# Kernel tuning notes

Hardware: AMD Instinct MI355X
Metric: run time of the kernel (lower is better)

## Reference

```python
import math
import jax, jax.numpy as jnp
import numpy as np

SCALING = 16.0 / 32.0  # alpha / rank


def real_fourier_orthogonal_multiply(c):
    """Vectorized equivalent of the per-frequency Python loop: build a complex
    spectrum from real Fourier coefficients and inverse-rfft along last dim."""
    n = c.shape[-1]
    sqrt_n = math.sqrt(n)
    pair_scale = math.sqrt(n / 2.0)
    max_f = (n - 1) // 2
    work = c.astype(jnp.float32)
    dc = (work[..., 0] * sqrt_n)[..., None].astype(jnp.complex64)
    cos = work[..., 1:1 + 2 * max_f:2] * pair_scale
    sin = work[..., 2:2 + 2 * max_f:2] * pair_scale
    mid = (cos - 1j * sin).astype(jnp.complex64)  # freqs 1..max_f
    parts = [dc, mid]
    if n % 2 == 0:
        parts.append((work[..., -1] * sqrt_n)[..., None].astype(jnp.complex64))
    spectrum = jnp.concatenate(parts, axis=-1)  # [..., n//2+1]
    return jnp.fft.irfft(spectrum, n=n, axis=-1).astype(c.dtype)


def setup_inputs() -> dict:
    key = jax.random.key(0)
    ks = jax.random.split(key, 9)
    B, S, D_in, D_out, R0, R1, E = 4, 2048, 4096, 4096, 32, 8, 3
    x = jax.random.normal(ks[0], (B, S, D_in), dtype=jnp.float32)
    W_base = jax.random.normal(ks[1], (D_out, D_in), dtype=jnp.float32) * 0.02
    b_base = jax.random.normal(ks[2], (D_out,), dtype=jnp.float32) * 0.02
    enc0 = jax.random.normal(ks[3], (R0, D_in), dtype=jnp.float32) * 0.02
    enc1 = jax.random.normal(ks[4], (R1, D_in), dtype=jnp.float32) * 0.02
    coefs0 = jax.random.normal(ks[5], (E, D_out, R0), dtype=jnp.float32) * 0.02
    coefs1 = jax.random.normal(ks[6], (E, D_out, R1), dtype=jnp.float32) * 0.02
    # sparse decoder masks (buffers in the torch module)
    mask0 = jax.random.randint(ks[7], (E, D_out, R0), 0, 2).astype(bool)
    mask1 = jax.random.randint(ks[8], (E, D_out, R1), 0, 2).astype(bool)
    return dict(x=x, W_base=W_base, b_base=b_base, enc0=enc0, enc1=enc1,
                coefs0=coefs0, coefs1=coefs1, mask0=mask0, mask1=mask1)


def reference(x, W_base, b_base, enc0, enc1, coefs0, coefs1, mask0, mask1):
    # base linear
    base = jnp.einsum('bsd,od->bso', x, W_base) + b_base
    # encoder blocks (shared across experts)
    e0 = jnp.einsum('bsd,rd->bsr', x, enc0)  # [B,S,R0]
    e1 = jnp.einsum('bsd,rd->bsr', x, enc1)  # [B,S,R1]
    # masked decoder blocks per expert, summed over blocks
    w0 = coefs0 * mask0.astype(coefs0.dtype)  # [E,O,R0]
    w1 = coefs1 * mask1.astype(coefs1.dtype)  # [E,O,R1]
    decoded = (jnp.einsum('bsr,eor->ebso', e0, w0)
               + jnp.einsum('bsr,eor->ebso', e1, w1))  # [E,B,S,O]
    transformed = real_fourier_orthogonal_multiply(decoded)
    update = transformed.sum(axis=0)  # sum over active experts
    return base + update * SCALING
```

## Files before the change

### kernel.cpp

```cpp
#include <hip/hip_runtime.h>

typedef __attribute__((ext_vector_type(2))) float f32x2;
typedef __attribute__((ext_vector_type(4))) float f32x4;
typedef __attribute__((ext_vector_type(16))) float f32x16;
typedef __attribute__((ext_vector_type(8))) short bf16x8;
typedef __attribute__((ext_vector_type(8))) unsigned short u16x8;

#define GL2LDS(g, l) __builtin_amdgcn_global_load_lds( \
    (const __attribute__((address_space(1))) void*)(g), \
    (__attribute__((address_space(3))) void*)(l), 16, 0, 0)

__device__ __forceinline__ unsigned short f2bf(float x) {
    union { float f; unsigned u; } v; v.f = x;
    unsigned r = (v.u + 0x7FFF + ((v.u >> 16) & 1)) >> 16;
    return (unsigned short)r;
}

__global__ __launch_bounds__(256) void k_prep(const float* __restrict__ c0,
                                              const float* __restrict__ c1,
                                              const int* __restrict__ m0,
                                              const int* __restrict__ m1,
                                              float* __restrict__ Wc,
                                              const float* __restrict__ x,
                                              unsigned short* __restrict__ xb) {
    int b = blockIdx.x;
    if (b < 640) {
        int idx = b * 256 + threadIdx.x;
        if (idx >= 4096 * 40) return;
        int o = idx / 40, c = idx % 40;
        float s = 0.f;
        if (c < 32) {
            #pragma unroll
            for (int e = 0; e < 3; ++e) {
                int i = (e * 4096 + o) * 32 + c;
                s += c0[i] * (m0[i] != 0 ? 1.f : 0.f);
            }
        } else {
            int r = c - 32;
            #pragma unroll
            for (int e = 0; e < 3; ++e) {
                int i = (e * 4096 + o) * 8 + r;
                s += c1[i] * (m1[i] != 0 ? 1.f : 0.f);
            }
        }
        Wc[idx] = s;
    } else {
        int idx = (b - 640) * 256 + threadIdx.x;
        f32x4 f0 = ((const f32x4*)x)[(size_t)idx * 2];
        f32x4 f1 = ((const f32x4*)x)[(size_t)idx * 2 + 1];
        u16x8 o;
        o[0] = f2bf(f0[0]); o[1] = f2bf(f0[1]); o[2] = f2bf(f0[2]); o[3] = f2bf(f0[3]);
        o[4] = f2bf(f1[0]); o[5] = f2bf(f1[1]); o[6] = f2bf(f1[2]); o[7] = f2bf(f1[3]);
        *(u16x8*)(xb + (size_t)idx * 8) = o;
    }
}

__global__ __launch_bounds__(256) void k_gmat(const float* __restrict__ Wc,
                                              float* __restrict__ G) {
    __shared__ float lds[10752];
    int tid = threadIdx.x;
    int t_base = blockIdx.x * 8;
    int f_slot = tid & 31;
    int tg = (tid >> 5) & 1;
    int rg = tid >> 6;
    float acc[4][10];
    #pragma unroll
    for (int a = 0; a < 4; ++a)
        #pragma unroll
        for (int b = 0; b < 10; ++b) acc[a][b] = 0.f;

    for (int ch = 0; ch < 16; ++ch) {
        __syncthreads();
        #pragma unroll
        for (int j = 0; j < 10; ++j) {
            int idx = tid + j * 256;
            int row = idx / 20;
            int v = idx % 20;
            int f = ch * 128 + row;
            f32x4 val = {0.f, 0.f, 0.f, 0.f};
            if (f >= 1) val = *(const f32x4*)(Wc + (2 * f - 1) * 40 + v * 4);
            *(f32x4*)(lds + row * 84 + v * 4) = val;
        }
        __syncthreads();
        #pragma unroll
        for (int j2 = 0; j2 < 4; ++j2) {
            int f_local = f_slot + 32 * j2;
            int f = ch * 128 + f_local;
            float cs[4], sn[4];
            #pragma unroll
            for (int tt = 0; tt < 4; ++tt) {
                int t = t_base + tg * 4 + tt;
                int ph = (f * t) & 4095;
                float rev = (float)ph * (1.0f / 4096.0f);
                cs[tt] = __builtin_amdgcn_cosf(rev);
                sn[tt] = __builtin_amdgcn_sinf(rev);
            }
            const float* Lc = lds + f_local * 84 + rg * 10;
            const float* Ls = Lc + 40;
            #pragma unroll
            for (int rr = 0; rr < 10; ++rr) {
                float wc = Lc[rr], ws = Ls[rr];
                #pragma unroll
                for (int tt = 0; tt < 4; ++tt)
                    acc[tt][rr] += cs[tt] * wc + sn[tt] * ws;
            }
        }
    }
    __syncthreads();
    #pragma unroll
    for (int tt = 0; tt < 4; ++tt)
        #pragma unroll
        for (int rr = 0; rr < 10; ++rr)
            lds[tid * 40 + tt * 10 + rr] = acc[tt][rr];
    __syncthreads();
    for (int oi = tid; oi < 320; oi += 256) {
        int t_local = oi / 40, rc = oi % 40;
        int tg2 = t_local >> 2, tsub = t_local & 3;
        int rg2 = rc / 10, rsub = rc % 10;
        float s = 0.f;
        #pragma unroll
        for (int fs = 0; fs < 32; ++fs)
            s += lds[(fs + tg2 * 32 + rg2 * 64) * 40 + tsub * 10 + rsub];
        int t = t_base + t_local;
        float dc = Wc[rc];
        float ny = Wc[4095 * 40 + rc];
        float sign = (t & 1) ? -1.f : 1.f;
        float g = 0.5f * (0.0220970869120796f * s + (dc + sign * ny) * (1.0f / 64.0f));
        G[t * 40 + rc] = g;
    }
}

__global__ __launch_bounds__(256) void k_wcomb(const float* __restrict__ Wb,
                                               const float* __restrict__ enc0,
                                               const float* __restrict__ enc1,
                                               const float* __restrict__ G,
                                               unsigned short* __restrict__ Wcb) {
    __shared__ float ldsE[40 * 256];
    __shared__ float ldsG[32 * 40];
    int tid = threadIdx.x;
    int d0 = blockIdx.x * 256;
    int t0 = blockIdx.y * 32;
    #pragma unroll
    for (int j = 0; j < 10; ++j) {
        int idx = tid + j * 256;
        int k = idx / 64, v = idx % 64;
        const float* src = (k < 32) ? (enc0 + (size_t)k * 4096) : (enc1 + (size_t)(k - 32) * 4096);
        *(f32x4*)(ldsE + k * 256 + v * 4) = *(const f32x4*)(src + d0 + v * 4);
    }
    #pragma unroll
    for (int j = 0; j < 5; ++j) {
        int idx = tid + j * 256;
        ldsG[idx] = G[(size_t)(t0 + idx / 40) * 40 + (idx % 40)];
    }
    __syncthreads();
    int dg = tid & 31, tg = tid >> 5;
    f32x2 a[4][4];
    #pragma unroll
    for (int s = 0; s < 4; ++s)
        #pragma unroll
        for (int tt = 0; tt < 4; ++tt) a[s][tt] = (f32x2){0.f, 0.f};
    #pragma unroll 8
    for (int r = 0; r < 40; ++r) {
        f32x2 e[4];
        #pragma unroll
        for (int s = 0; s < 4; ++s)
            e[s] = *(const f32x2*)(ldsE + r * 256 + s * 64 + dg * 2);
        #pragma unroll
        for (int tt = 0; tt < 4; ++tt) {
            float g = ldsG[(tg * 4 + tt) * 40 + r];
            #pragma unroll
            for (int s = 0; s < 4; ++s)
                a[s][tt] += g * e[s];
        }
    }
    #pragma unroll
    for (int tt = 0; tt < 4; ++tt) {
        int t = t0 + tg * 4 + tt;
        #pragma unroll
        for (int s = 0; s < 4; ++s) {
            int d = d0 + s * 64 + dg * 2;
            f32x2 wv = *(const f32x2*)(Wb + (size_t)t * 4096 + d);
            f32x2 rv = a[s][tt] + wv;
            unsigned short lo = f2bf(rv[0]), hi = f2bf(rv[1]);
            *(unsigned*)(Wcb + (size_t)t * 4096 + d) = (unsigned)lo | ((unsigned)hi << 16);
        }
    }
}

__global__ __launch_bounds__(256) void k_gemm(const unsigned short* __restrict__ A,
                                              const unsigned short* __restrict__ B,
                                              const float* __restrict__ bias,
                                              float* __restrict__ C) {
    __shared__ short As[128 * 64];
    __shared__ short Bs[128 * 64];
    int tid = threadIdx.x;
    int lane = tid & 63, w = tid >> 6;
    int m0 = blockIdx.y * 128, n0 = blockIdx.x * 128;
    int wm = w >> 1, wn = w & 1;
    int col = lane & 31;
    int hi = lane >> 5;
    int sw = col & 7;

    f32x16 acc[2][2];
    #pragma unroll
    for (int i = 0; i < 2; ++i)
        #pragma unroll
        for (int j = 0; j < 2; ++j)
            #pragma unroll
            for (int r = 0; r < 16; ++r) acc[i][j][r] = 0.f;

    int rw = lane >> 3;
    int cg = (lane & 7) ^ rw;
    const unsigned short* Ab = A + (size_t)(m0 + w * 32 + rw) * 4096 + cg * 8;
    const unsigned short* Bb = B + (size_t)(n0 + w * 32 + rw) * 4096 + cg * 8;

    int aoff0 = (wm * 64 + col) * 64;
    int boff0 = (wn * 64 + col) * 64;

    for (int kt = 0; kt < 4096; kt += 64) {
        __syncthreads();
        #pragma unroll
        for (int i = 0; i < 4; ++i) {
            GL2LDS(Ab + (size_t)(i * 8) * 4096 + kt, &As[(w * 32 + i * 8) * 64]);
            GL2LDS(Bb + (size_t)(i * 8) * 4096 + kt, &Bs[(w * 32 + i * 8) * 64]);
        }
        __syncthreads();
        #pragma unroll
        for (int ks = 0; ks < 4; ++ks) {
            int co = ((ks * 2 + hi) ^ sw) * 8;
            bf16x8 a0 = *(const bf16x8*)&As[aoff0 + co];
            bf16x8 a1 = *(const bf16x8*)&As[aoff0 + 32 * 64 + co];
            bf16x8 b0 = *(const bf16x8*)&Bs[boff0 + co];
            bf16x8 b1 = *(const bf16x8*)&Bs[boff0 + 32 * 64 + co];
            acc[0][0] = __builtin_amdgcn_mfma_f32_32x32x16_bf16(a0, b0, acc[0][0], 0, 0, 0);
            acc[0][1] = __builtin_amdgcn_mfma_f32_32x32x16_bf16(a0, b1, acc[0][1], 0, 0, 0);
            acc[1][0] = __builtin_amdgcn_mfma_f32_32x32x16_bf16(a1, b0, acc[1][0], 0, 0, 0);
            acc[1][1] = __builtin_amdgcn_mfma_f32_32x32x16_bf16(a1, b1, acc[1][1], 0, 0, 0);
        }
    }

    float bv[2];
    #pragma unroll
    for (int j = 0; j < 2; ++j) bv[j] = bias[n0 + wn * 64 + j * 32 + col];
    #pragma unroll
    for (int i = 0; i < 2; ++i)
        #pragma unroll
        for (int r = 0; r < 16; ++r) {
            int row = m0 + wm * 64 + i * 32 + (r & 3) + 8 * (r >> 2) + 4 * hi;
            float* crow = C + (size_t)row * 4096 + n0 + wn * 64 + col;
            crow[0]  = acc[i][0][r] + bv[0];
            crow[32] = acc[i][1][r] + bv[1];
        }
}

extern "C" void kernel_launch(void* const* d_in, const int* in_sizes, int n_in,
                              void* d_out, int out_size, void* d_ws, size_t ws_size,
                              hipStream_t stream) {
    const float* x   = (const float*)d_in[0];
    const float* Wb  = (const float*)d_in[1];
    const float* bb  = (const float*)d_in[2];
    const float* e0  = (const float*)d_in[3];
    const float* e1  = (const float*)d_in[4];
    const float* c0  = (const float*)d_in[5];
    const float* c1  = (const float*)d_in[6];
    const int*   m0  = (const int*)d_in[7];
    const int*   m1  = (const int*)d_in[8];
    float* out = (float*)d_out;

    char* ws = (char*)d_ws;
    unsigned short* xb  = (unsigned short*)ws;
    float* Wc           = (float*)(ws + 67108864);
    float* G            = (float*)(ws + 67764224);
    unsigned short* Wcb = (unsigned short*)(ws + 68419584);

    k_prep <<<17024, 256, 0, stream>>>(c0, c1, m0, m1, Wc, x, xb);
    k_gmat <<<512, 256, 0, stream>>>(Wc, G);
    k_wcomb<<<dim3(16, 128), 256, 0, stream>>>(Wb, e0, e1, G, Wcb);
    k_gemm <<<dim3(32, 64), 256, 0, stream>>>(xb, Wcb, bb, out);
}
```

Baseline: 631.2 us.

## Rewrite bf16 GEMM with 256x256 tiles, double-buffered LDS and interleaved MFMA phases

```diff
diff --git a/kernel.cpp b/kernel.cpp
--- a/kernel.cpp
+++ b/kernel.cpp
@@ -187,70 +187,133 @@
     }
 }
 
-__global__ __launch_bounds__(256) void k_gemm(const unsigned short* __restrict__ A,
-                                              const unsigned short* __restrict__ B,
-                                              const float* __restrict__ bias,
-                                              float* __restrict__ C) {
-    __shared__ short As[128 * 64];
-    __shared__ short Bs[128 * 64];
-    int tid = threadIdx.x;
-    int lane = tid & 63, w = tid >> 6;
-    int m0 = blockIdx.y * 128, n0 = blockIdx.x * 128;
-    int wm = w >> 1, wn = w & 1;
-    int col = lane & 31;
-    int hi = lane >> 5;
-    int sw = col & 7;
-
-    f32x16 acc[2][2];
-    #pragma unroll
-    for (int i = 0; i < 2; ++i)
-        #pragma unroll
-        for (int j = 0; j < 2; ++j)
-            #pragma unroll
-            for (int r = 0; r < 16; ++r) acc[i][j][r] = 0.f;
-
-    int rw = lane >> 3;
-    int cg = (lane & 7) ^ rw;
-    const unsigned short* Ab = A + (size_t)(m0 + w * 32 + rw) * 4096 + cg * 8;
-    const unsigned short* Bb = B + (size_t)(n0 + w * 32 + rw) * 4096 + cg * 8;
-
-    int aoff0 = (wm * 64 + col) * 64;
-    int boff0 = (wn * 64 + col) * 64;
-
-    for (int kt = 0; kt < 4096; kt += 64) {
-        __syncthreads();
-        #pragma unroll
-        for (int i = 0; i < 4; ++i) {
-            GL2LDS(Ab + (size_t)(i * 8) * 4096 + kt, &As[(w * 32 + i * 8) * 64]);
-            GL2LDS(Bb + (size_t)(i * 8) * 4096 + kt, &Bs[(w * 32 + i * 8) * 64]);
-        }
-        __syncthreads();
-        #pragma unroll
-        for (int ks = 0; ks < 4; ++ks) {
-            int co = ((ks * 2 + hi) ^ sw) * 8;
-            bf16x8 a0 = *(const bf16x8*)&As[aoff0 + co];
-            bf16x8 a1 = *(const bf16x8*)&As[aoff0 + 32 * 64 + co];
-            bf16x8 b0 = *(const bf16x8*)&Bs[boff0 + co];
-            bf16x8 b1 = *(const bf16x8*)&Bs[boff0 + 32 * 64 + co];
-            acc[0][0] = __builtin_amdgcn_mfma_f32_32x32x16_bf16(a0, b0, acc[0][0], 0, 0, 0);
-            acc[0][1] = __builtin_amdgcn_mfma_f32_32x32x16_bf16(a0, b1, acc[0][1], 0, 0, 0);
-            acc[1][0] = __builtin_amdgcn_mfma_f32_32x32x16_bf16(a1, b0, acc[1][0], 0, 0, 0);
-            acc[1][1] = __builtin_amdgcn_mfma_f32_32x32x16_bf16(a1, b1, acc[1][1], 0, 0, 0);
-        }
-    }
-
-    float bv[2];
-    #pragma unroll
-    for (int j = 0; j < 2; ++j) bv[j] = bias[n0 + wn * 64 + j * 32 + col];
-    #pragma unroll
-    for (int i = 0; i < 2; ++i)
-        #pragma unroll
-        for (int r = 0; r < 16; ++r) {
-            int row = m0 + wm * 64 + i * 32 + (r & 3) + 8 * (r >> 2) + 4 * hi;
-            float* crow = C + (size_t)row * 4096 + n0 + wn * 64 + col;
-            crow[0]  = acc[i][0][r] + bv[0];
-            crow[32] = acc[i][1][r] + bv[1];
-        }
+__global__ __launch_bounds__(512, 2) void k_gemm(const unsigned short* __restrict__ A,
+                                                 const unsigned short* __restrict__ B,
+                                                 const float* __restrict__ bias,
+                                                 float* __restrict__ C) {
+    __shared__ __align__(16) short As[2][256 * 64];
+    __shared__ __align__(16) short Bs[2][256 * 64];
+    const int tid = threadIdx.x;
+    const int lane = tid & 63, w = tid >> 6;
+    const int wm = w >> 2, wn = w & 3;
+    const int col = lane & 31, hi = lane >> 5;
+    const int sw = col & 7;
+
+    int bid = blockIdx.x;
+    int swz = (bid & 7) * 64 + (bid >> 3);
+    int m0 = (swz >> 4) * 256;
+    int n0 = (swz & 15) * 256;
+
+    const int srow = w * 8 + (lane >> 3);
+    const int scg  = (lane & 7) ^ ((lane >> 3) & 7);
+    const unsigned short* Ag = A + (size_t)(m0 + srow) * 4096 + scg * 8;
+    const unsigned short* Bg = B + (size_t)(n0 + srow) * 4096 + scg * 8;
+
+#define STAGE(buf, kt) do { \
+    _Pragma("unroll") \
+    for (int c = 0; c < 4; ++c) { \
+        GL2LDS(Ag + (size_t)(c * 64) * 4096 + (kt), &As[buf][(c * 64 + w * 8) * 64]); \
+        GL2LDS(Bg + (size_t)(c * 64) * 4096 + (kt), &Bs[buf][(c * 64 + w * 8) * 64]); \
+    } \
+} while (0)
+
+    int aoff[4], boff[2], co[4];
+    #pragma unroll
+    for (int mf = 0; mf < 4; ++mf) aoff[mf] = (wm * 128 + mf * 32 + col) * 64;
+    #pragma unroll
+    for (int nf = 0; nf < 2; ++nf) boff[nf] = (wn * 64 + nf * 32 + col) * 64;
+    #pragma unroll
+    for (int ks = 0; ks < 4; ++ks) co[ks] = ((ks * 2 + hi) ^ sw) * 8;
+
+    f32x16 acc[4][2];
+    #pragma unroll
+    for (int mf = 0; mf < 4; ++mf)
+        #pragma unroll
+        for (int nf = 0; nf < 2; ++nf)
+            #pragma unroll
+            for (int r = 0; r < 16; ++r) acc[mf][nf][r] = 0.f;
+
+    STAGE(0, 0);
+    STAGE(1, 64);
+    asm volatile("s_waitcnt vmcnt(8)\n\ts_barrier" ::: "memory");
+
+    for (int t = 0; t < 64; ++t) {
+        const int cur = t & 1;
+        bf16x8 aLo[2][4], b0[4];
+        #pragma unroll
+        for (int ks = 0; ks < 4; ++ks) {
+            aLo[0][ks] = *(const bf16x8*)&As[cur][aoff[0] + co[ks]];
+            aLo[1][ks] = *(const bf16x8*)&As[cur][aoff[1] + co[ks]];
+            b0[ks]     = *(const bf16x8*)&Bs[cur][boff[0] + co[ks]];
+        }
+        asm volatile("s_barrier" ::: "memory");
+        __builtin_amdgcn_s_setprio(1);
+        #pragma unroll
+        for (int ks = 0; ks < 4; ++ks) {
+            acc[0][0] = __builtin_amdgcn_mfma_f32_32x32x16_bf16(aLo[0][ks], b0[ks], acc[0][0], 0, 0, 0);
+            acc[1][0] = __builtin_amdgcn_mfma_f32_32x32x16_bf16(aLo[1][ks], b0[ks], acc[1][0], 0, 0, 0);
+        }
+        __builtin_amdgcn_s_setprio(0);
+        asm volatile("s_barrier" ::: "memory");
+        bf16x8 aHi[2][4];
+        #pragma unroll
+        for (int ks = 0; ks < 4; ++ks) {
+            aHi[0][ks] = *(const bf16x8*)&As[cur][aoff[2] + co[ks]];
+            aHi[1][ks] = *(const bf16x8*)&As[cur][aoff[3] + co[ks]];
+        }
+        asm volatile("s_barrier" ::: "memory");
+        __builtin_amdgcn_s_setprio(1);
+        #pragma unroll
+        for (int ks = 0; ks < 4; ++ks) {
+            acc[2][0] = __builtin_amdgcn_mfma_f32_32x32x16_bf16(aHi[0][ks], b0[ks], acc[2][0], 0, 0, 0);
+            acc[3][0] = __builtin_amdgcn_mfma_f32_32x32x16_bf16(aHi[1][ks], b0[ks], acc[3][0], 0, 0, 0);
+        }
+        __builtin_amdgcn_s_setprio(0);
+        asm volatile("s_barrier" ::: "memory");
+        bf16x8 b1[4];
+        #pragma unroll
+        for (int ks = 0; ks < 4; ++ks)
+            b1[ks] = *(const bf16x8*)&Bs[cur][boff[1] + co[ks]];
+        asm volatile("s_barrier" ::: "memory");
+        __builtin_amdgcn_s_setprio(1);
+        #pragma unroll
+        for (int ks = 0; ks < 4; ++ks) {
+            acc[2][1] = __builtin_amdgcn_mfma_f32_32x32x16_bf16(aHi[0][ks], b1[ks], acc[2][1], 0, 0, 0);
+            acc[3][1] = __builtin_amdgcn_mfma_f32_32x32x16_bf16(aHi[1][ks], b1[ks], acc[3][1], 0, 0, 0);
+        }
+        __builtin_amdgcn_s_setprio(0);
+        asm volatile("s_barrier" ::: "memory");
+        if (t + 2 < 64) STAGE(cur, (t + 2) * 64);
+        asm volatile("s_barrier" ::: "memory");
+        __builtin_amdgcn_s_setprio(1);
+        #pragma unroll
+        for (int ks = 0; ks < 4; ++ks) {
+            acc[0][1] = __builtin_amdgcn_mfma_f32_32x32x16_bf16(aLo[0][ks], b1[ks], acc[0][1], 0, 0, 0);
+            acc[1][1] = __builtin_amdgcn_mfma_f32_32x32x16_bf16(aLo[1][ks], b1[ks], acc[1][1], 0, 0, 0);
+        }
+        __builtin_amdgcn_s_setprio(0);
+        if (t + 2 < 64) {
+            asm volatile("s_waitcnt vmcnt(8)\n\ts_barrier" ::: "memory");
+        } else if (t + 1 < 64) {
+            asm volatile("s_waitcnt vmcnt(0)\n\ts_barrier" ::: "memory");
+        } else {
+            asm volatile("s_barrier" ::: "memory");
+        }
+    }
+#undef STAGE
+
+    #pragma unroll
+    for (int nf = 0; nf < 2; ++nf) {
+        float bv = bias[n0 + wn * 64 + nf * 32 + col];
+        #pragma unroll
+        for (int mf = 0; mf < 4; ++mf) {
+            #pragma unroll
+            for (int r = 0; r < 16; ++r) {
+                int row = m0 + wm * 128 + mf * 32 + (r & 3) + 8 * (r >> 2) + 4 * hi;
+                C[(size_t)row * 4096 + n0 + wn * 64 + nf * 32 + col] = acc[mf][nf][r] + bv;
+            }
+        }
+    }
 }
 
 extern "C" void kernel_launch(void* const* d_in, const int* in_sizes, int n_in,
@@ -276,5 +339,5 @@
     k_prep <<<17024, 256, 0, stream>>>(c0, c1, m0, m1, Wc, x, xb);
     k_gmat <<<512, 256, 0, stream>>>(Wc, G);
     k_wcomb<<<dim3(16, 128), 256, 0, stream>>>(Wb, e0, e1, G, Wcb);
-    k_gemm <<<dim3(32, 64), 256, 0, stream>>>(xb, Wcb, bb, out);
-}
+    k_gemm <<<512, 512, 0, stream>>>(xb, Wcb, bb, out);
+}
```

Result: slower. 686.9 us (+8.8%).
